# Kernel optimization log

Hardware: AMD Instinct MI355X
Metric: run time of the kernel (lower is better)

Reference implementation:

```python
import jax, jax.numpy as jnp
import numpy as np

B, S, DIM, H = 1, 4096, 1024, 16
HEAD_DIM = DIM // H
ROPE_THETA = 10000.0
LN_EPS = 1e-5


def _rope_cos_sin(seq_len, dim, theta):
    # frequencies over the FULL model dim (rope applied before head split, as in source)
    inv_freq = 1.0 / (theta ** (jnp.arange(0, dim, 2, dtype=jnp.float32) / dim))  # (dim/2,)
    ang = jnp.arange(seq_len, dtype=jnp.float32)[:, None] * inv_freq[None, :]     # (S, dim/2)
    cos = jnp.concatenate([jnp.cos(ang), jnp.cos(ang)], axis=-1)                  # (S, dim)
    sin = jnp.concatenate([jnp.sin(ang), jnp.sin(ang)], axis=-1)
    return cos, sin


def _rotate_half(x):
    d = x.shape[-1] // 2
    return jnp.concatenate([-x[..., d:], x[..., :d]], axis=-1)


def _apply_rope(x, cos, sin):
    # x: (B, S, dim); cos/sin: (S, dim)
    return x * cos[None] + _rotate_half(x) * sin[None]


def setup_inputs() -> dict:
    key = jax.random.key(0)
    ks = jax.random.split(key, 5)
    sc = 1.0 / np.sqrt(DIM)
    return {
        "x": jax.random.normal(ks[0], (B, S, DIM), dtype=jnp.float32),
        "Wqkv": jax.random.normal(ks[1], (DIM, 3 * DIM), dtype=jnp.float32) * sc,
        "bqkv": jax.random.normal(ks[2], (3 * DIM,), dtype=jnp.float32) * 0.01,
        "Wo": jax.random.normal(ks[3], (DIM, DIM), dtype=jnp.float32) * sc,
        "bo": jax.random.normal(ks[4], (DIM,), dtype=jnp.float32) * 0.01,
        "gamma": jnp.ones((DIM,), dtype=jnp.float32),
        "beta": jnp.zeros((DIM,), dtype=jnp.float32),
    }


def reference(x, Wqkv, bqkv, Wo, bo, gamma, beta):
    b, s, d = x.shape
    qkv = x @ Wqkv + bqkv                      # (B, S, 3*dim)
    q, k, v = jnp.split(qkv, 3, axis=-1)       # each (B, S, dim)
    cos, sin = _rope_cos_sin(s, d, ROPE_THETA)
    q = _apply_rope(q, cos, sin)
    k = _apply_rope(k, cos, sin)
    # split heads
    q = q.reshape(b, s, H, HEAD_DIM)
    k = k.reshape(b, s, H, HEAD_DIM)
    v = v.reshape(b, s, H, HEAD_DIM)
    scale = 1.0 / np.sqrt(HEAD_DIM)
    scores = jnp.einsum('bqhd,bkhd->bhqk', q, k) * scale  # (B, H, S, S)
    causal = jnp.triu(jnp.ones((s, s), dtype=bool), k=1)
    scores = jnp.where(causal[None, None], -jnp.inf, scores)
    attn = jax.nn.softmax(scores, axis=-1)
    out = jnp.einsum('bhqk,bkhd->bqhd', attn, v).reshape(b, s, d)
    out = out @ Wo + bo
    # LayerNorm (dropout is identity in eval mode)
    mu = jnp.mean(out, axis=-1, keepdims=True)
    var = jnp.mean(jnp.square(out - mu), axis=-1, keepdims=True)
    return (out - mu) * jax.lax.rsqrt(var + LN_EPS) * gamma + beta
```

## Files before the change

### kernel.cpp

```cpp
#include <hip/hip_runtime.h>
#include <cstdint>
#include <cstddef>

#define S_LEN 4096
#define DIM   1024
#define NH    16
#define HD    64
#define QKV_N 3072
#define NSPLIT 2

typedef __attribute__((ext_vector_type(8))) short short8;
typedef __attribute__((ext_vector_type(4))) float f32x4;
typedef __attribute__((ext_vector_type(16))) float f32x16;
typedef __attribute__((ext_vector_type(4))) unsigned short ushort4v;
typedef __attribute__((ext_vector_type(2))) unsigned int uint2v;
typedef __attribute__((ext_vector_type(4))) unsigned int uint4v;

__device__ inline unsigned short f2bf(float x) {
    unsigned int u = __builtin_bit_cast(unsigned int, x);
    u += 0x7fffu + ((u >> 16) & 1u);
    return (unsigned short)(u >> 16);
}
__device__ inline float bf2f(unsigned short u) {
    return __builtin_bit_cast(float, (unsigned int)u << 16);
}
__device__ inline unsigned int pack2_bf16_rh(float lo, float hi) {
    unsigned int a = __builtin_bit_cast(unsigned int, lo) + 0x8000u;
    unsigned int b = __builtin_bit_cast(unsigned int, hi) + 0x8000u;
    return __builtin_amdgcn_perm(b, a, 0x07060302u);
}

__device__ inline void gl_lds16(const void* g, void* l) {
    __builtin_amdgcn_global_load_lds(
        (const __attribute__((address_space(1))) void*)g,
        (__attribute__((address_space(3))) void*)l, 16, 0, 0);
}

template <bool BF16OUT>
__global__ __launch_bounds__(256) void gemm_mfma_kernel(
    const unsigned short* __restrict__ A,
    const unsigned short* __restrict__ Bt,
    const float* __restrict__ bias,
    void* __restrict__ Cv,
    int M, int N, int K)
{
    __shared__ unsigned short As[128 * 32];
    __shared__ unsigned short Bs[128 * 32];

    const int t    = threadIdx.x;
    const int w    = t >> 6;
    const int lane = t & 63;
    const int ln   = lane & 15;
    const int quad = lane >> 4;
    const int bm   = blockIdx.y * 128;
    const int bn   = blockIdx.x * 128;
    const int wm   = (w & 1) * 64;
    const int wn   = (w >> 1) * 64;

    f32x4 acc[4][4];
#pragma unroll
    for (int i = 0; i < 4; ++i)
#pragma unroll
        for (int j = 0; j < 4; ++j) acc[i][j] = (f32x4){0.f, 0.f, 0.f, 0.f};

    const int lr = lane >> 2;
    const int lc = (lane & 3) * 8;
    const unsigned short* ga = A  + (size_t)(bm + w * 32 + lr) * K + lc;
    const unsigned short* gb = Bt + (size_t)(bn + w * 32 + lr) * K + lc;
    unsigned short* la = &As[(w * 32) * 32];
    unsigned short* lb = &Bs[(w * 32) * 32];

    for (int k0 = 0; k0 < K; k0 += 32) {
        gl_lds16(ga,            la);
        gl_lds16(ga + 16 * K,   la + 16 * 32);
        gl_lds16(gb,            lb);
        gl_lds16(gb + 16 * K,   lb + 16 * 32);
        ga += 32; gb += 32;
        __syncthreads();

        short8 af[4], bf[4];
#pragma unroll
        for (int i = 0; i < 4; ++i)
            af[i] = *(const short8*)&As[(wm + i * 16 + ln) * 32 + quad * 8];
#pragma unroll
        for (int j = 0; j < 4; ++j)
            bf[j] = *(const short8*)&Bs[(wn + j * 16 + ln) * 32 + quad * 8];
#pragma unroll
        for (int i = 0; i < 4; ++i)
#pragma unroll
            for (int j = 0; j < 4; ++j)
                acc[i][j] = __builtin_amdgcn_mfma_f32_16x16x32_bf16(af[i], bf[j], acc[i][j], 0, 0, 0);
        __syncthreads();
    }

#pragma unroll
    for (int j = 0; j < 4; ++j) {
        const int col = bn + wn + j * 16 + ln;
        const float bv = bias[col];
#pragma unroll
        for (int i = 0; i < 4; ++i) {
            const int row0 = bm + wm + i * 16 + quad * 4;
#pragma unroll
            for (int r = 0; r < 4; ++r) {
                const float v = acc[i][j][r] + bv;
                if (BF16OUT)
                    ((unsigned short*)Cv)[(size_t)(row0 + r) * N + col] = f2bf(v);
                else
                    ((float*)Cv)[(size_t)(row0 + r) * N + col] = v;
            }
        }
    }
}

__global__ __launch_bounds__(256) void gemm_mfma64_kernel(
    const unsigned short* __restrict__ A,
    const unsigned short* __restrict__ Bt,
    const float* __restrict__ bias,
    float* __restrict__ C,
    int M, int N, int K)
{
    __shared__ unsigned short As[64 * 32];
    __shared__ unsigned short Bs[128 * 32];

    const int t    = threadIdx.x;
    const int w    = t >> 6;
    const int lane = t & 63;
    const int ln   = lane & 15;
    const int quad = lane >> 4;
    const int bm   = blockIdx.y * 64;
    const int bn   = blockIdx.x * 128;
    const int wm   = (w >> 1) * 32;
    const int wn   = (w & 1) * 64;

    f32x4 acc[2][4];
#pragma unroll
    for (int i = 0; i < 2; ++i)
#pragma unroll
        for (int j = 0; j < 4; ++j) acc[i][j] = (f32x4){0.f, 0.f, 0.f, 0.f};

    const int lr = lane >> 2;
    const int lc = (lane & 3) * 8;
    const unsigned short* ga = A  + (size_t)(bm + w * 16 + lr) * K + lc;
    const unsigned short* gb = Bt + (size_t)(bn + w * 32 + lr) * K + lc;
    unsigned short* la = &As[(w * 16) * 32];
    unsigned short* lb = &Bs[(w * 32) * 32];

    for (int k0 = 0; k0 < K; k0 += 32) {
        gl_lds16(ga,            la);
        gl_lds16(gb,            lb);
        gl_lds16(gb + 16 * K,   lb + 16 * 32);
        ga += 32; gb += 32;
        __syncthreads();

        short8 af[2], bf[4];
#pragma unroll
        for (int i = 0; i < 2; ++i)
            af[i] = *(const short8*)&As[(wm + i * 16 + ln) * 32 + quad * 8];
#pragma unroll
        for (int j = 0; j < 4; ++j)
            bf[j] = *(const short8*)&Bs[(wn + j * 16 + ln) * 32 + quad * 8];
#pragma unroll
        for (int i = 0; i < 2; ++i)
#pragma unroll
            for (int j = 0; j < 4; ++j)
                acc[i][j] = __builtin_amdgcn_mfma_f32_16x16x32_bf16(af[i], bf[j], acc[i][j], 0, 0, 0);
        __syncthreads();
    }

#pragma unroll
    for (int j = 0; j < 4; ++j) {
        const int col = bn + wn + j * 16 + ln;
        const float bv = bias[col];
#pragma unroll
        for (int i = 0; i < 2; ++i) {
            const int row0 = bm + wm + i * 16 + quad * 4;
#pragma unroll
            for (int r = 0; r < 4; ++r)
                C[(size_t)(row0 + r) * N + col] = acc[i][j][r] + bv;
        }
    }
}

__global__ __launch_bounds__(256) void prep1_kernel(
    const float* __restrict__ x, unsigned short* __restrict__ xb,
    const float* __restrict__ Wqkv, unsigned short* __restrict__ WqkvT,
    const float* __restrict__ Wo, unsigned short* __restrict__ WoT)
{
    __shared__ unsigned short L[64][72];
    const int b = blockIdx.x;
    const int t = threadIdx.x;

    if (b < 2048) {
        const size_t i = ((size_t)b * 256 + t) * 8;
        float4 a = *(const float4*)(x + i);
        float4 c = *(const float4*)(x + i + 4);
        short8 p = { (short)f2bf(a.x), (short)f2bf(a.y), (short)f2bf(a.z), (short)f2bf(a.w),
                     (short)f2bf(c.x), (short)f2bf(c.y), (short)f2bf(c.z), (short)f2bf(c.w) };
        *(short8*)(xb + i) = p;
        return;
    }
    const float* W;
    unsigned short* Wt;
    int N, n0, k0;
    if (b < 2816) {
        const int wb = b - 2048;
        W = Wqkv; Wt = WqkvT; N = QKV_N;
        n0 = (wb % 48) * 64; k0 = (wb / 48) * 64;
    } else {
        const int wb = b - 2816;
        W = Wo; Wt = WoT; N = DIM;
        n0 = (wb & 15) * 64; k0 = (wb >> 4) * 64;
    }
    const int kr = t >> 2, cb = (t & 3) * 16;
    const float* wp = W + (size_t)(k0 + kr) * N + n0 + cb;
#pragma unroll
    for (int u = 0; u < 16; u += 4) {
        float4 v = *(const float4*)(wp + u);
        ushort4v p = { f2bf(v.x), f2bf(v.y), f2bf(v.z), f2bf(v.w) };
        *(ushort4v*)&L[kr][cb + u] = p;
    }
    __syncthreads();
    const int nr = t >> 2, kb = (t & 3) * 16;
    short8 lo, hi;
#pragma unroll
    for (int u = 0; u < 8; ++u) lo[u] = (short)L[kb + u][nr];
#pragma unroll
    for (int u = 0; u < 8; ++u) hi[u] = (short)L[kb + 8 + u][nr];
    unsigned short* op = Wt + (size_t)(n0 + nr) * 1024 + k0 + kb;
    *(short8*)op       = lo;
    *(short8*)(op + 8) = hi;
}

__global__ __launch_bounds__(256) void prep2_kernel(
    const unsigned short* __restrict__ qkvb,
    unsigned short* __restrict__ Qb,
    unsigned short* __restrict__ Kb,
    unsigned short* __restrict__ Vt)
{
    __shared__ unsigned short L[64][72];
    const int b = blockIdx.x;
    const int t = threadIdx.x;

    if (b < 2048) {
        const int idx = b * 256 + t;
        const int j   = (idx & 127) * 4;
        const int s   = idx >> 7;
        const unsigned short* row = qkvb + (size_t)s * QKV_N;
        unsigned short* qo = Qb + (size_t)s * DIM;
        unsigned short* ko = Kb + (size_t)s * DIM;
        const float sf = (float)s;
        const float QSCALE = 0.18033688011112042f;
        const float C1 = -0.025952563241307517f;
        const float INV2PI = 0.15915494309189535f;

        float cs[4], sn[4];
#pragma unroll
        for (int e = 0; e < 4; ++e) {
            const float invf2pi = exp2f((float)(j + e) * C1) * INV2PI;
            float rev = sf * invf2pi;
            rev -= floorf(rev);
            sn[e] = __builtin_amdgcn_sinf(rev);
            cs[e] = __builtin_amdgcn_cosf(rev);
        }
        ushort4v q1 = *(const ushort4v*)(row + j);
        ushort4v q2 = *(const ushort4v*)(row + 512 + j);
        ushort4v k1 = *(const ushort4v*)(row + DIM + j);
        ushort4v k2 = *(const ushort4v*)(row + DIM + 512 + j);
        ushort4v qa, qb4, ka, kb4;
#pragma unroll
        for (int e = 0; e < 4; ++e) {
            const float x1 = bf2f(q1[e]), x2 = bf2f(q2[e]);
            const float y1 = bf2f(k1[e]), y2 = bf2f(k2[e]);
            qa[e]  = f2bf((x1 * cs[e] - x2 * sn[e]) * QSCALE);
            qb4[e] = f2bf((x2 * cs[e] + x1 * sn[e]) * QSCALE);
            ka[e]  = f2bf(y1 * cs[e] - y2 * sn[e]);
            kb4[e] = f2bf(y2 * cs[e] + y1 * sn[e]);
        }
        *(ushort4v*)(qo + j)       = qa;
        *(ushort4v*)(qo + 512 + j) = qb4;
        *(ushort4v*)(ko + j)       = ka;
        *(ushort4v*)(ko + 512 + j) = kb4;
        return;
    }

    const int vb = b - 2048;
    const int c0 = (vb & 15) * 64;
    const int bs = (vb >> 4) * 64;
    const int sl = t >> 2, cb = (t & 3) * 16;
    const unsigned short* vp = qkvb + (size_t)(bs + sl) * QKV_N + 2 * DIM + c0 + cb;
    *(short8*)&L[sl][cb]     = *(const short8*)vp;
    *(short8*)&L[sl][cb + 8] = *(const short8*)(vp + 8);
    __syncthreads();
    const int cl = t >> 2, sb = (t & 3) * 16;
    short8 lo, hi;
#pragma unroll
    for (int u = 0; u < 8; ++u) lo[u] = (short)L[sb + u][cl];
#pragma unroll
    for (int u = 0; u < 8; ++u) hi[u] = (short)L[sb + 8 + u][cl];
    unsigned short* op = Vt + (size_t)(c0 + cl) * S_LEN + bs + sb;
    *(short8*)op       = lo;
    *(short8*)(op + 8) = hi;
}

__global__ __launch_bounds__(256) void attn_mfma_kernel(
    const unsigned short* __restrict__ Qb,
    const unsigned short* __restrict__ Kb,
    const unsigned short* __restrict__ Vt,
    unsigned short* __restrict__ Opb,
    float* __restrict__ lp)
{
    __shared__ unsigned short Ks[2][64 * 64];
    __shared__ unsigned short Vs[2][64 * 64];

    const int t    = threadIdx.x;
    const int w    = t >> 6;
    const int lane = t & 63;
    const int r31  = lane & 31;
    const int hi   = lane >> 5;
    const int p    = blockIdx.x;
    const int spl  = blockIdx.y;
    const int h    = blockIdx.z;

    const int srow  = t >> 2;
    const int sch   = (t & 3) * 2;
    const int ssw   = srow & 7;
    const int soff0 = srow * 64 + ((sch ^ ssw) << 3);
    const int soff1 = srow * 64 + (((sch + 1) ^ ssw) << 3);

    const int rA = r31 * 64;
    const int sw = r31 & 7;

#pragma unroll
    for (int phase = 0; phase < 2; ++phase) {
        const int qt  = phase == 0 ? (31 - p) : p;
        const int q0  = qt * 128;
        const int nkt = 2 * qt + 2;
        const int kt_begin = (nkt * spl) / NSPLIT;
        const int kt_end   = (nkt * (spl + 1)) / NSPLIT;

        short8 qf[4];
        {
            const unsigned short* qp = Qb + (size_t)(q0 + w * 32 + r31) * DIM + h * HD + hi * 8;
#pragma unroll
            for (int kk = 0; kk < 4; ++kk) qf[kk] = *(const short8*)(qp + kk * 16);
        }

        f32x16 o0 = {}, o1 = {};
        float lrow = 0.f;

        short8 kr0, kr1, vr0, vr1;
        {
            const int k0 = kt_begin * 64;
            const unsigned short* kp = Kb + (size_t)(k0 + srow) * DIM + h * HD + sch * 8;
            kr0 = *(const short8*)kp;  kr1 = *(const short8*)(kp + 8);
            const unsigned short* vp = Vt + (size_t)(h * HD + srow) * S_LEN + k0 + sch * 8;
            vr0 = *(const short8*)vp;  vr1 = *(const short8*)(vp + 8);
        }
        __syncthreads();

        for (int kt = kt_begin; kt < kt_end; ++kt) {
            const int buf = (kt - kt_begin) & 1;
            unsigned short* ks = &Ks[buf][0];
            unsigned short* vs = &Vs[buf][0];
            *(short8*)&ks[soff0] = kr0;
            *(short8*)&ks[soff1] = kr1;
            *(short8*)&vs[soff0] = vr0;
            *(short8*)&vs[soff1] = vr1;
            if (kt + 1 < kt_end) {
                const int k1 = (kt + 1) * 64;
                const unsigned short* kp = Kb + (size_t)(k1 + srow) * DIM + h * HD + sch * 8;
                kr0 = *(const short8*)kp;  kr1 = *(const short8*)(kp + 8);
                const unsigned short* vp = Vt + (size_t)(h * HD + srow) * S_LEN + k1 + sch * 8;
                vr0 = *(const short8*)vp;  vr1 = *(const short8*)(vp + 8);
            }
            __syncthreads();

            f32x16 s0 = {}, s1 = {};
            __builtin_amdgcn_s_setprio(1);
#pragma unroll
            for (int kk = 0; kk < 4; ++kk) {
                const int co = (((kk * 2 + hi) ^ sw) << 3);
                short8 kf0 = *(const short8*)&ks[rA + co];
                short8 kf1 = *(const short8*)&ks[rA + 2048 + co];
                s0 = __builtin_amdgcn_mfma_f32_32x32x16_bf16(kf0, qf[kk], s0, 0, 0, 0);
                s1 = __builtin_amdgcn_mfma_f32_32x32x16_bf16(kf1, qf[kk], s1, 0, 0, 0);
            }
            __builtin_amdgcn_s_setprio(0);

            if (kt >= nkt - 2) {
                const int qg = q0 + w * 32 + r31;
                const int kb = kt * 64 + 4 * hi;
#pragma unroll
                for (int g = 0; g < 4; ++g)
#pragma unroll
                    for (int a = 0; a < 4; ++a) {
                        const int keyl = kb + a + 8 * g;
                        if (keyl > qg)      s0[4 * g + a] = -1e30f;
                        if (keyl + 32 > qg) s1[4 * g + a] = -1e30f;
                    }
            }

            unsigned int pd0[8], pd1[8];
            float ps = 0.f;
#pragma unroll
            for (int g = 0; g < 4; ++g) {
                const float a0 = __builtin_amdgcn_exp2f(s0[4 * g + 0]);
                const float a1 = __builtin_amdgcn_exp2f(s0[4 * g + 1]);
                const float a2 = __builtin_amdgcn_exp2f(s0[4 * g + 2]);
                const float a3 = __builtin_amdgcn_exp2f(s0[4 * g + 3]);
                const float b0 = __builtin_amdgcn_exp2f(s1[4 * g + 0]);
                const float b1 = __builtin_amdgcn_exp2f(s1[4 * g + 1]);
                const float b2 = __builtin_amdgcn_exp2f(s1[4 * g + 2]);
                const float b3 = __builtin_amdgcn_exp2f(s1[4 * g + 3]);
                ps += ((a0 + a1) + (a2 + a3)) + ((b0 + b1) + (b2 + b3));
                pd0[2 * g]     = pack2_bf16_rh(a0, a1);
                pd0[2 * g + 1] = pack2_bf16_rh(a2, a3);
                pd1[2 * g]     = pack2_bf16_rh(b0, b1);
                pd1[2 * g + 1] = pack2_bf16_rh(b2, b3);
            }
            ps += __shfl_xor(ps, 32);
            lrow += ps;

#pragma unroll
            for (int w16 = 0; w16 < 4; ++w16) {
                const int lw = w16 & 1;
                unsigned int a0, b0, a1, b1;
                if (w16 < 2) { a0 = pd0[4 * lw];     b0 = pd0[4 * lw + 2];
                               a1 = pd0[4 * lw + 1]; b1 = pd0[4 * lw + 3]; }
                else         { a0 = pd1[4 * lw];     b0 = pd1[4 * lw + 2];
                               a1 = pd1[4 * lw + 1]; b1 = pd1[4 * lw + 3]; }
                asm("v_permlane32_swap_b32 %0, %1" : "+v"(a0), "+v"(b0));
                asm("v_permlane32_swap_b32 %0, %1" : "+v"(a1), "+v"(b1));
                const uint4v frw = { a0, a1, b0, b1 };
                const short8 pf = __builtin_bit_cast(short8, frw);
                const int co = (((w16 * 2 + hi) ^ sw) << 3);
                short8 vf0 = *(const short8*)&vs[rA + co];
                short8 vf1 = *(const short8*)&vs[rA + 2048 + co];
                __builtin_amdgcn_s_setprio(1);
                o0 = __builtin_amdgcn_mfma_f32_32x32x16_bf16(vf0, pf, o0, 0, 0, 0);
                o1 = __builtin_amdgcn_mfma_f32_32x32x16_bf16(vf1, pf, o1, 0, 0, 0);
                __builtin_amdgcn_s_setprio(0);
            }
        }

        {
            unsigned short* op = Opb + ((size_t)spl * S_LEN + q0 + w * 32 + r31) * DIM + h * HD + hi * 4;
#pragma unroll
            for (int g = 0; g < 4; ++g) {
                ushort4v v0 = { f2bf(o0[4 * g + 0]), f2bf(o0[4 * g + 1]),
                                f2bf(o0[4 * g + 2]), f2bf(o0[4 * g + 3]) };
                ushort4v v1 = { f2bf(o1[4 * g + 0]), f2bf(o1[4 * g + 1]),
                                f2bf(o1[4 * g + 2]), f2bf(o1[4 * g + 3]) };
                *(ushort4v*)(op + g * 8)      = v0;
                *(ushort4v*)(op + 32 + g * 8) = v1;
            }
            if (hi == 0)
                lp[((size_t)spl * NH + h) * S_LEN + q0 + w * 32 + r31] = lrow;
        }
    }
}

__global__ __launch_bounds__(256) void combine_kernel(
    const unsigned short* __restrict__ Opb, const float* __restrict__ lp,
    unsigned short* __restrict__ attnb)
{
    const int row = blockIdx.x;
    const int t   = threadIdx.x;
    const int d   = t * 4;
    const int h   = t >> 4;
    float acc[4] = {0.f, 0.f, 0.f, 0.f};
    float l = 0.f;
#pragma unroll
    for (int s = 0; s < NSPLIT; ++s) {
        ushort4v a = *(const ushort4v*)&Opb[((size_t)s * S_LEN + row) * DIM + d];
#pragma unroll
        for (int e = 0; e < 4; ++e) acc[e] += bf2f(a[e]);
        l += lp[((size_t)s * NH + h) * S_LEN + row];
    }
    const float inv = 1.0f / l;
    ushort4v o;
#pragma unroll
    for (int e = 0; e < 4; ++e) o[e] = f2bf(acc[e] * inv);
    *(ushort4v*)&attnb[(size_t)row * DIM + d] = o;
}

__global__ __launch_bounds__(256) void ln_kernel(
    const float* __restrict__ in, const float* __restrict__ gamma,
    const float* __restrict__ beta, float* __restrict__ out)
{
    const int row = blockIdx.x;
    const int t = threadIdx.x;
    const float4 v = *(const float4*)&in[(size_t)row * DIM + t * 4];
    float s  = v.x + v.y + v.z + v.w;
    float sq = v.x * v.x + v.y * v.y + v.z * v.z + v.w * v.w;
#pragma unroll
    for (int off = 1; off < 64; off <<= 1) {
        s  += __shfl_xor(s, off);
        sq += __shfl_xor(sq, off);
    }
    __shared__ float red[8];
    const int wv = t >> 6, ln = t & 63;
    if (ln == 0) { red[wv] = s; red[4 + wv] = sq; }
    __syncthreads();
    s  = red[0] + red[1] + red[2] + red[3];
    sq = red[4] + red[5] + red[6] + red[7];
    const float mu  = s * (1.0f / DIM);
    const float var = sq * (1.0f / DIM) - mu * mu;
    const float rs  = rsqrtf(var + 1e-5f);
    const float4 g = *(const float4*)&gamma[t * 4];
    const float4 b = *(const float4*)&beta[t * 4];
    float4 o = { (v.x - mu) * rs * g.x + b.x,
                 (v.y - mu) * rs * g.y + b.y,
                 (v.z - mu) * rs * g.z + b.z,
                 (v.w - mu) * rs * g.w + b.w };
    *(float4*)&out[(size_t)row * DIM + t * 4] = o;
}

extern "C" void kernel_launch(void* const* d_in, const int* in_sizes, int n_in,
                              void* d_out, int out_size, void* d_ws, size_t ws_size,
                              hipStream_t stream)
{
    const float* x     = (const float*)d_in[0];
    const float* Wqkv  = (const float*)d_in[1];
    const float* bqkv  = (const float*)d_in[2];
    const float* Wo    = (const float*)d_in[3];
    const float* bo    = (const float*)d_in[4];
    const float* gamma = (const float*)d_in[5];
    const float* beta  = (const float*)d_in[6];
    float* out = (float*)d_out;

    char* base = (char*)d_ws;
    unsigned short* qkvb  = (unsigned short*)base;
    unsigned short* attnb = (unsigned short*)base;
    unsigned short* Opb   = (unsigned short*)(base + (size_t)8 * 1024 * 1024);
    float* proj = (float*)(base + (size_t)8 * 1024 * 1024);
    float* lp   = (float*)(base + (size_t)40 * 1024 * 1024);
    unsigned short* Qb    = (unsigned short*)(base + (size_t)48 * 1024 * 1024);
    unsigned short* Kb    = (unsigned short*)(base + (size_t)56 * 1024 * 1024);
    unsigned short* Vt    = (unsigned short*)(base + (size_t)64 * 1024 * 1024);
    unsigned short* xb    = (unsigned short*)(base + (size_t)72 * 1024 * 1024);
    unsigned short* WqkvT = (unsigned short*)(base + (size_t)80 * 1024 * 1024);
    unsigned short* WoT   = (unsigned short*)(base + (size_t)86 * 1024 * 1024);

    prep1_kernel<<<3072, 256, 0, stream>>>(x, xb, Wqkv, WqkvT, Wo, WoT);

    gemm_mfma_kernel<true><<<dim3(QKV_N / 128, S_LEN / 128), 256, 0, stream>>>(
        xb, WqkvT, bqkv, qkvb, S_LEN, QKV_N, DIM);

    prep2_kernel<<<3072, 256, 0, stream>>>(qkvb, Qb, Kb, Vt);

    attn_mfma_kernel<<<dim3(16, NSPLIT, NH), 256, 0, stream>>>(Qb, Kb, Vt, Opb, lp);

    combine_kernel<<<S_LEN, 256, 0, stream>>>(Opb, lp, attnb);

    gemm_mfma64_kernel<<<dim3(DIM / 128, S_LEN / 64), 256, 0, stream>>>(
        attnb, WoT, bo, proj, S_LEN, DIM, DIM);

    ln_kernel<<<S_LEN, 256, 0, stream>>>(proj, gamma, beta, out);
}
```

Baseline: 228.2 us.

## Split-K output projection with 128x128 tiles, fuse bias into LayerNorm, raise attention splits

The output projection now uses a 128x128-tile split-K GEMM over two K halves and writes two fp32 partial buffers. LayerNorm sums the partials and adds the output bias, replacing the previous 64x128 bias-adding GEMM. Attention KV splits rise from 2 to 4, so the attention grid has more blocks for load balance. In exchange the code moves more partial-result data through memory in the combine and LayerNorm stages.

Result: slower. 242.0 us (+6.0%).

```diff
diff --git a/kernel.cpp b/kernel.cpp
--- a/kernel.cpp
+++ b/kernel.cpp
@@ -7,7 +7,7 @@
 #define NH    16
 #define HD    64
 #define QKV_N 3072
-#define NSPLIT 2
+#define NSPLIT 4
 
 typedef __attribute__((ext_vector_type(8))) short short8;
 typedef __attribute__((ext_vector_type(4))) float f32x4;
@@ -36,12 +36,11 @@
         (__attribute__((address_space(3))) void*)l, 16, 0, 0);
 }
 
-template <bool BF16OUT>
 __global__ __launch_bounds__(256) void gemm_mfma_kernel(
     const unsigned short* __restrict__ A,
     const unsigned short* __restrict__ Bt,
     const float* __restrict__ bias,
-    void* __restrict__ Cv,
+    unsigned short* __restrict__ C,
     int M, int N, int K)
 {
     __shared__ unsigned short As[128 * 32];
@@ -101,25 +100,19 @@
         for (int i = 0; i < 4; ++i) {
             const int row0 = bm + wm + i * 16 + quad * 4;
 #pragma unroll
-            for (int r = 0; r < 4; ++r) {
-                const float v = acc[i][j][r] + bv;
-                if (BF16OUT)
-                    ((unsigned short*)Cv)[(size_t)(row0 + r) * N + col] = f2bf(v);
-                else
-                    ((float*)Cv)[(size_t)(row0 + r) * N + col] = v;
-            }
-        }
-    }
-}
-
-__global__ __launch_bounds__(256) void gemm_mfma64_kernel(
+            for (int r = 0; r < 4; ++r)
+                C[(size_t)(row0 + r) * N + col] = f2bf(acc[i][j][r] + bv);
+        }
+    }
+}
+
+__global__ __launch_bounds__(256) void gemm_mfma_splitk_kernel(
     const unsigned short* __restrict__ A,
     const unsigned short* __restrict__ Bt,
-    const float* __restrict__ bias,
-    float* __restrict__ C,
+    float* __restrict__ P,
     int M, int N, int K)
 {
-    __shared__ unsigned short As[64 * 32];
+    __shared__ unsigned short As[128 * 32];
     __shared__ unsigned short Bs[128 * 32];
 
     const int t    = threadIdx.x;
@@ -127,56 +120,59 @@
     const int lane = t & 63;
     const int ln   = lane & 15;
     const int quad = lane >> 4;
-    const int bm   = blockIdx.y * 64;
+    const int bm   = blockIdx.y * 128;
     const int bn   = blockIdx.x * 128;
-    const int wm   = (w >> 1) * 32;
-    const int wn   = (w & 1) * 64;
-
-    f32x4 acc[2][4];
-#pragma unroll
-    for (int i = 0; i < 2; ++i)
+    const int z    = blockIdx.z;
+    const int wm   = (w & 1) * 64;
+    const int wn   = (w >> 1) * 64;
+    const int kh   = K >> 1;
+
+    f32x4 acc[4][4];
+#pragma unroll
+    for (int i = 0; i < 4; ++i)
 #pragma unroll
         for (int j = 0; j < 4; ++j) acc[i][j] = (f32x4){0.f, 0.f, 0.f, 0.f};
 
     const int lr = lane >> 2;
     const int lc = (lane & 3) * 8;
-    const unsigned short* ga = A  + (size_t)(bm + w * 16 + lr) * K + lc;
-    const unsigned short* gb = Bt + (size_t)(bn + w * 32 + lr) * K + lc;
-    unsigned short* la = &As[(w * 16) * 32];
+    const unsigned short* ga = A  + (size_t)(bm + w * 32 + lr) * K + z * kh + lc;
+    const unsigned short* gb = Bt + (size_t)(bn + w * 32 + lr) * K + z * kh + lc;
+    unsigned short* la = &As[(w * 32) * 32];
     unsigned short* lb = &Bs[(w * 32) * 32];
 
-    for (int k0 = 0; k0 < K; k0 += 32) {
+    for (int k0 = 0; k0 < kh; k0 += 32) {
         gl_lds16(ga,            la);
+        gl_lds16(ga + 16 * K,   la + 16 * 32);
         gl_lds16(gb,            lb);
         gl_lds16(gb + 16 * K,   lb + 16 * 32);
         ga += 32; gb += 32;
         __syncthreads();
 
-        short8 af[2], bf[4];
-#pragma unroll
-        for (int i = 0; i < 2; ++i)
+        short8 af[4], bf[4];
+#pragma unroll
+        for (int i = 0; i < 4; ++i)
             af[i] = *(const short8*)&As[(wm + i * 16 + ln) * 32 + quad * 8];
 #pragma unroll
         for (int j = 0; j < 4; ++j)
             bf[j] = *(const short8*)&Bs[(wn + j * 16 + ln) * 32 + quad * 8];
 #pragma unroll
-        for (int i = 0; i < 2; ++i)
+        for (int i = 0; i < 4; ++i)
 #pragma unroll
             for (int j = 0; j < 4; ++j)
                 acc[i][j] = __builtin_amdgcn_mfma_f32_16x16x32_bf16(af[i], bf[j], acc[i][j], 0, 0, 0);
         __syncthreads();
     }
 
+    float* Pz = P + (size_t)z * M * N;
 #pragma unroll
     for (int j = 0; j < 4; ++j) {
         const int col = bn + wn + j * 16 + ln;
-        const float bv = bias[col];
-#pragma unroll
-        for (int i = 0; i < 2; ++i) {
+#pragma unroll
+        for (int i = 0; i < 4; ++i) {
             const int row0 = bm + wm + i * 16 + quad * 4;
 #pragma unroll
             for (int r = 0; r < 4; ++r)
-                C[(size_t)(row0 + r) * N + col] = acc[i][j][r] + bv;
+                Pz[(size_t)(row0 + r) * N + col] = acc[i][j][r];
         }
     }
 }
@@ -485,12 +481,17 @@
 }
 
 __global__ __launch_bounds__(256) void ln_kernel(
-    const float* __restrict__ in, const float* __restrict__ gamma,
+    const float* __restrict__ p0, const float* __restrict__ p1,
+    const float* __restrict__ bo, const float* __restrict__ gamma,
     const float* __restrict__ beta, float* __restrict__ out)
 {
     const int row = blockIdx.x;
     const int t = threadIdx.x;
-    const float4 v = *(const float4*)&in[(size_t)row * DIM + t * 4];
+    const float4 a = *(const float4*)&p0[(size_t)row * DIM + t * 4];
+    const float4 c = *(const float4*)&p1[(size_t)row * DIM + t * 4];
+    const float4 bb = *(const float4*)&bo[t * 4];
+    const float4 v = { a.x + c.x + bb.x, a.y + c.y + bb.y,
+                       a.z + c.z + bb.z, a.w + c.w + bb.w };
     float s  = v.x + v.y + v.z + v.w;
     float sq = v.x * v.x + v.y * v.y + v.z * v.z + v.w * v.w;
 #pragma unroll
@@ -544,7 +545,7 @@
 
     prep1_kernel<<<3072, 256, 0, stream>>>(x, xb, Wqkv, WqkvT, Wo, WoT);
 
-    gemm_mfma_kernel<true><<<dim3(QKV_N / 128, S_LEN / 128), 256, 0, stream>>>(
+    gemm_mfma_kernel<<<dim3(QKV_N / 128, S_LEN / 128), 256, 0, stream>>>(
         xb, WqkvT, bqkv, qkvb, S_LEN, QKV_N, DIM);
 
     prep2_kernel<<<3072, 256, 0, stream>>>(qkvb, Qb, Kb, Vt);
@@ -553,8 +554,9 @@
 
     combine_kernel<<<S_LEN, 256, 0, stream>>>(Opb, lp, attnb);
 
-    gemm_mfma64_kernel<<<dim3(DIM / 128, S_LEN / 64), 256, 0, stream>>>(
-        attnb, WoT, bo, proj, S_LEN, DIM, DIM);
-
-    ln_kernel<<<S_LEN, 256, 0, stream>>>(proj, gamma, beta, out);
-}
+    gemm_mfma_splitk_kernel<<<dim3(DIM / 128, S_LEN / 128, 2), 256, 0, stream>>>(
+        attnb, WoT, proj, S_LEN, DIM, DIM);
+
+    ln_kernel<<<S_LEN, 256, 0, stream>>>(proj, proj + (size_t)S_LEN * DIM, bo,
+                                         gamma, beta, out);
+}
```

## Remap block IDs for XCD-aware L2 locality and drop MFMA setprio hints

Applied to the files above, without the earlier changes.

Both GEMMs and the attention kernel now use 1-D grids and remap the block index so that consecutive blocks landing on the same XCD (blockIdx mod 8) work on contiguous tiles or on the same head. The goal is to raise L2 reuse of shared A/B tiles and K/V data within each XCD's private L2 on MI355X. The s_setprio bracketing around the MFMA loops in attention is also removed. The GEMM template is reduced to the bf16 output path only. The remapping assumes the tile counts divide evenly by 8, and dropping setprio may change how wavefronts interleave.

Measured after the change: 225.5 us. About the same (-1.2%).

```diff
diff --git a/kernel.cpp b/kernel.cpp
--- a/kernel.cpp
+++ b/kernel.cpp
@@ -13,7 +13,6 @@
 typedef __attribute__((ext_vector_type(4))) float f32x4;
 typedef __attribute__((ext_vector_type(16))) float f32x16;
 typedef __attribute__((ext_vector_type(4))) unsigned short ushort4v;
-typedef __attribute__((ext_vector_type(2))) unsigned int uint2v;
 typedef __attribute__((ext_vector_type(4))) unsigned int uint4v;
 
 __device__ inline unsigned short f2bf(float x) {
@@ -36,24 +35,26 @@
         (__attribute__((address_space(3))) void*)l, 16, 0, 0);
 }
 
-template <bool BF16OUT>
 __global__ __launch_bounds__(256) void gemm_mfma_kernel(
     const unsigned short* __restrict__ A,
     const unsigned short* __restrict__ Bt,
     const float* __restrict__ bias,
-    void* __restrict__ Cv,
+    unsigned short* __restrict__ C,
     int M, int N, int K)
 {
     __shared__ unsigned short As[128 * 32];
     __shared__ unsigned short Bs[128 * 32];
 
+    const int nbn  = N >> 7;
+    const int per  = (M >> 7) * nbn / 8;
+    const int tid  = (blockIdx.x & 7) * per + (blockIdx.x >> 3);
     const int t    = threadIdx.x;
     const int w    = t >> 6;
     const int lane = t & 63;
     const int ln   = lane & 15;
     const int quad = lane >> 4;
-    const int bm   = blockIdx.y * 128;
-    const int bn   = blockIdx.x * 128;
+    const int bm   = (tid / nbn) * 128;
+    const int bn   = (tid % nbn) * 128;
     const int wm   = (w & 1) * 64;
     const int wn   = (w >> 1) * 64;
 
@@ -101,13 +102,8 @@
         for (int i = 0; i < 4; ++i) {
             const int row0 = bm + wm + i * 16 + quad * 4;
 #pragma unroll
-            for (int r = 0; r < 4; ++r) {
-                const float v = acc[i][j][r] + bv;
-                if (BF16OUT)
-                    ((unsigned short*)Cv)[(size_t)(row0 + r) * N + col] = f2bf(v);
-                else
-                    ((float*)Cv)[(size_t)(row0 + r) * N + col] = v;
-            }
+            for (int r = 0; r < 4; ++r)
+                C[(size_t)(row0 + r) * N + col] = f2bf(acc[i][j][r] + bv);
         }
     }
 }
@@ -122,13 +118,16 @@
     __shared__ unsigned short As[64 * 32];
     __shared__ unsigned short Bs[128 * 32];
 
+    const int nbn  = N >> 7;
+    const int per  = (M >> 6) * nbn / 8;
+    const int tid  = (blockIdx.x & 7) * per + (blockIdx.x >> 3);
     const int t    = threadIdx.x;
     const int w    = t >> 6;
     const int lane = t & 63;
     const int ln   = lane & 15;
     const int quad = lane >> 4;
-    const int bm   = blockIdx.y * 64;
-    const int bn   = blockIdx.x * 128;
+    const int bm   = (tid / nbn) * 64;
+    const int bn   = (tid % nbn) * 128;
     const int wm   = (w >> 1) * 32;
     const int wn   = (w & 1) * 64;
 
@@ -317,9 +316,11 @@
     const int lane = t & 63;
     const int r31  = lane & 31;
     const int hi   = lane >> 5;
-    const int p    = blockIdx.x;
-    const int spl  = blockIdx.y;
-    const int h    = blockIdx.z;
+    const int b    = blockIdx.x;
+    const int slot = b >> 3;
+    const int h    = (b & 7) + 8 * (slot >> 5);
+    const int p    = slot & 15;
+    const int spl  = (slot >> 4) & 1;
 
     const int srow  = t >> 2;
     const int sch   = (t & 3) * 2;
@@ -376,7 +377,6 @@
             __syncthreads();
 
             f32x16 s0 = {}, s1 = {};
-            __builtin_amdgcn_s_setprio(1);
 #pragma unroll
             for (int kk = 0; kk < 4; ++kk) {
                 const int co = (((kk * 2 + hi) ^ sw) << 3);
@@ -385,7 +385,6 @@
                 s0 = __builtin_amdgcn_mfma_f32_32x32x16_bf16(kf0, qf[kk], s0, 0, 0, 0);
                 s1 = __builtin_amdgcn_mfma_f32_32x32x16_bf16(kf1, qf[kk], s1, 0, 0, 0);
             }
-            __builtin_amdgcn_s_setprio(0);
 
             if (kt >= nkt - 2) {
                 const int qg = q0 + w * 32 + r31;
@@ -436,10 +435,8 @@
                 const int co = (((w16 * 2 + hi) ^ sw) << 3);
                 short8 vf0 = *(const short8*)&vs[rA + co];
                 short8 vf1 = *(const short8*)&vs[rA + 2048 + co];
-                __builtin_amdgcn_s_setprio(1);
                 o0 = __builtin_amdgcn_mfma_f32_32x32x16_bf16(vf0, pf, o0, 0, 0, 0);
                 o1 = __builtin_amdgcn_mfma_f32_32x32x16_bf16(vf1, pf, o1, 0, 0, 0);
-                __builtin_amdgcn_s_setprio(0);
             }
         }
 
@@ -544,16 +541,16 @@
 
     prep1_kernel<<<3072, 256, 0, stream>>>(x, xb, Wqkv, WqkvT, Wo, WoT);
 
-    gemm_mfma_kernel<true><<<dim3(QKV_N / 128, S_LEN / 128), 256, 0, stream>>>(
+    gemm_mfma_kernel<<<768, 256, 0, stream>>>(
         xb, WqkvT, bqkv, qkvb, S_LEN, QKV_N, DIM);
 
     prep2_kernel<<<3072, 256, 0, stream>>>(qkvb, Qb, Kb, Vt);
 
-    attn_mfma_kernel<<<dim3(16, NSPLIT, NH), 256, 0, stream>>>(Qb, Kb, Vt, Opb, lp);
+    attn_mfma_kernel<<<16 * NSPLIT * NH, 256, 0, stream>>>(Qb, Kb, Vt, Opb, lp);
 
     combine_kernel<<<S_LEN, 256, 0, stream>>>(Opb, lp, attnb);
 
-    gemm_mfma64_kernel<<<dim3(DIM / 128, S_LEN / 64), 256, 0, stream>>>(
+    gemm_mfma64_kernel<<<512, 256, 0, stream>>>(
         attnb, WoT, bo, proj, S_LEN, DIM, DIM);
 
     ln_kernel<<<S_LEN, 256, 0, stream>>>(proj, gamma, beta, out);
```
